# Optimization experiments

Measured on AMD Instinct MI355X. Metric: run time of the kernel, lower is better.

Reference implementation:

```python
import jax, jax.numpy as jnp
import numpy as np

N_NODES = 100000
N_EDGES = 1600000
K = 48

def setup_inputs() -> dict:
    key = jax.random.key(0)
    ks = jax.random.split(key, 6)
    x = jax.random.normal(ks[0], (N_NODES, K), dtype=jnp.float32)
    pos_edge_index = jax.random.randint(ks[1], (2, N_EDGES), 0, N_NODES, dtype=jnp.int64)
    neg_edge_index = jax.random.randint(ks[2], (2, N_EDGES), 0, N_NODES, dtype=jnp.int64)
    # nn.Linear-style init (uniform +-1/sqrt(fan_in))
    lim1 = 1.0 / np.sqrt(3 * K)
    W1 = jax.random.uniform(ks[3], (3 * K, 16), minval=-lim1, maxval=lim1, dtype=jnp.float32)
    b1 = jnp.zeros((16,), dtype=jnp.float32)
    lim2 = 1.0 / np.sqrt(16)
    W2 = jax.random.uniform(ks[4], (16, K), minval=-lim2, maxval=lim2, dtype=jnp.float32)
    b2 = jnp.zeros((K,), dtype=jnp.float32)
    return {"x": x, "pos_edge_index": pos_edge_index, "neg_edge_index": neg_edge_index,
            "W1": W1, "b1": b1, "W2": W2, "b2": b2}

def _scatter_add_mp(x, edge_index):
    # PyG MessagePassing(aggr='add'), message = x_j:
    # gather source-node features and scatter-add into target nodes.
    src, dst = edge_index[0], edge_index[1]
    msgs = x[src]  # [E, k]
    return jax.ops.segment_sum(msgs, dst, num_segments=x.shape[0])  # [N, k]

def reference(x, pos_edge_index, neg_edge_index, W1, b1, W2, b2):
    x_pos = _scatter_add_mp(x, pos_edge_index)
    x_neg = _scatter_add_mp(x, neg_edge_index)
    out_cat = jnp.concatenate([x, x_pos, x_neg], axis=1)  # [N, 3k]
    h = jnp.tanh(out_cat @ W1 + b1)                        # [N, 16]
    C = h @ W2 + b2                                        # [N, k]
    return jax.nn.softmax(C, axis=1)
```

## Files before the change

### kernel.cpp

```cpp
#include <hip/hip_runtime.h>
#include <hip/hip_fp16.h>
#include <math.h>

#define NN 100000
#define NE 1600000
#define KF 48
#define NEDGE_ALL (2 * NE)

#define BKT_NODES 128
#define NBKT_PER  782
#define NBKT      1564
#define PACK_EPB  16384
#define STG_HALF  8192
#define NPB       196
#define OT2       1566
#define CAP2      2432
#define KSTG      10

typedef _Float16 half2v __attribute__((ext_vector_type(2)));
typedef _Float16 half4v __attribute__((ext_vector_type(4)));
typedef _Float16 half8v __attribute__((ext_vector_type(8)));

#if defined(__has_builtin)
#if __has_builtin(__builtin_amdgcn_fdot2)
#define HAVE_FDOT2 1
#endif
#endif

__device__ __forceinline__ void acc_pair(float& ax, float& ay, half2v v)
{
#ifdef HAVE_FDOT2
    ax = __builtin_amdgcn_fdot2(v, (half2v){(_Float16)1.f, (_Float16)0.f}, ax, false);
    ay = __builtin_amdgcn_fdot2(v, (half2v){(_Float16)0.f, (_Float16)1.f}, ay, false);
#else
    ax += (float)v.x;
    ay += (float)v.y;
#endif
}

__global__ __launch_bounds__(512) void pack_kernel(
    const float* __restrict__ x,
    const int* __restrict__ ei_pos,
    const int* __restrict__ ei_neg,
    const float* __restrict__ W1,
    const float* __restrict__ b1,
    unsigned short* __restrict__ offT,
    unsigned* __restrict__ plist,
    float* __restrict__ za,
    __half* __restrict__ zbh,
    __half* __restrict__ zch)
{
    __shared__ int cnt[NBKT];
    __shared__ int ps[391];
    __shared__ unsigned stage[STG_HALF];
    __shared__ float sW1[144 * 16];
    __shared__ float sb1[16];

    const int t = threadIdx.x;
    for (int i = t; i < 144 * 16; i += 512) sW1[i] = W1[i];
    if (t < 16) sb1[t] = b1[t];
    for (int i = t; i < NBKT; i += 512) cnt[i] = 0;
    __syncthreads();

    {
        const int n = blockIdx.x * 512 + t;
        if (n < NN + 2) {
            float aA[16], aB[16], aC[16];
#pragma unroll
            for (int j = 0; j < 16; ++j) { aA[j] = sb1[j]; aB[j] = 0.f; aC[j] = 0.f; }
            if (n < NN) {
                const float4* __restrict__ x4 = (const float4*)(x + (long)n * KF);
                for (int i4 = 0; i4 < 12; ++i4) {
                    float4 v = x4[i4];
                    float vv[4] = {v.x, v.y, v.z, v.w};
#pragma unroll
                    for (int c = 0; c < 4; ++c) {
                        const int f = i4 * 4 + c;
                        const float* wA = &sW1[f * 16];
                        const float* wB = &sW1[(48 + f) * 16];
                        const float* wC = &sW1[(96 + f) * 16];
                        const float s = vv[c];
#pragma unroll
                        for (int j = 0; j < 16; ++j) {
                            aA[j] += s * wA[j];
                            aB[j] += s * wB[j];
                            aC[j] += s * wC[j];
                        }
                    }
                }
                float4* za4 = (float4*)(za + (long)n * 16);
#pragma unroll
                for (int j4 = 0; j4 < 4; ++j4)
                    za4[j4] = make_float4(aA[4*j4], aA[4*j4+1], aA[4*j4+2], aA[4*j4+3]);
            }
            half8v hb0, hb1, hc0, hc1;
#pragma unroll
            for (int j = 0; j < 8; ++j) {
                hb0[j] = (_Float16)aB[j];     hb1[j] = (_Float16)aB[8 + j];
                hc0[j] = (_Float16)aC[j];     hc1[j] = (_Float16)aC[8 + j];
            }
            half8v* zb8 = (half8v*)zbh;
            half8v* zc8 = (half8v*)zch;
            zb8[(long)n * 2 + 0] = hb0;  zb8[(long)n * 2 + 1] = hb1;
            zc8[(long)n * 2 + 0] = hc0;  zc8[(long)n * 2 + 1] = hc1;
        }
    }

    unsigned pk[32];
    int bk[32];
    const int blockBase = blockIdx.x * PACK_EPB;
#pragma unroll
    for (int j = 0; j < 32; ++j) {
        int e = blockBase + j * 512 + t;
        bk[j] = -1;
        if (e < NEDGE_ALL) {
            int list = e >= NE;
            int ee = list ? e - NE : e;
            const int* ei = list ? ei_neg : ei_pos;
            int src = ei[ee];
            int dst = ei[NE + ee];
            int b = list * NBKT_PER + (dst >> 7);
            bk[j] = b;
            pk[j] = ((unsigned)(dst & 127) << 17) | (unsigned)src;
            atomicAdd(&cnt[b], 1);
        }
    }
    __syncthreads();

    int s0 = 0, s1 = 0, s2 = 0, s3 = 0;
    if (t < 391) {
        s0 = cnt[4 * t]; s1 = cnt[4 * t + 1]; s2 = cnt[4 * t + 2]; s3 = cnt[4 * t + 3];
        ps[t] = s0 + s1 + s2 + s3;
    }
    __syncthreads();
    for (int d = 1; d < 391; d <<= 1) {
        int v = (t < 391 && t >= d) ? ps[t - d] : 0;
        __syncthreads();
        if (t < 391) ps[t] += v;
        __syncthreads();
    }
    unsigned short* myrow = offT + (long)blockIdx.x * OT2;
    if (t < 391) {
        int base = t ? ps[t - 1] : 0;
        int o0 = base, o1 = o0 + s0, o2 = o1 + s1, o3 = o2 + s2;
        myrow[4 * t]     = (unsigned short)o0;
        myrow[4 * t + 1] = (unsigned short)o1;
        myrow[4 * t + 2] = (unsigned short)o2;
        myrow[4 * t + 3] = (unsigned short)o3;
        cnt[4 * t] = o0; cnt[4 * t + 1] = o1; cnt[4 * t + 2] = o2; cnt[4 * t + 3] = o3;
    }
    if (t == 390) myrow[NBKT] = (unsigned short)ps[390];
    __syncthreads();

#pragma unroll
    for (int j = 0; j < 32; ++j) {
        if (bk[j] >= 0)
            bk[j] = atomicAdd(&cnt[bk[j]], 1);
    }

#pragma unroll
    for (int j = 0; j < 32; ++j) {
        if (bk[j] >= 0 && bk[j] < STG_HALF)
            stage[bk[j]] = pk[j];
    }
    __syncthreads();
    {
        const uint4* __restrict__ st4 = (const uint4*)stage;
        uint4* __restrict__ out4 = (uint4*)(plist + (long)blockIdx.x * PACK_EPB);
#pragma unroll
        for (int j = 0; j < 4; ++j)
            out4[j * 512 + t] = st4[j * 512 + t];
    }
    __syncthreads();

#pragma unroll
    for (int j = 0; j < 32; ++j) {
        if (bk[j] >= STG_HALF)
            stage[bk[j] - STG_HALF] = pk[j];
    }
    __syncthreads();
    {
        const uint4* __restrict__ st4 = (const uint4*)stage;
        uint4* __restrict__ out4 = (uint4*)(plist + (long)blockIdx.x * PACK_EPB + STG_HALF);
#pragma unroll
        for (int j = 0; j < 4; ++j)
            out4[j * 512 + t] = st4[j * 512 + t];
    }
}

__global__ __launch_bounds__(256) void gather_kernel(
    const __half* __restrict__ zbh,
    const __half* __restrict__ zch,
    const unsigned* __restrict__ plist,
    const unsigned short* __restrict__ offT,
    float* __restrict__ hpos,
    float* __restrict__ hneg)
{
    __shared__ unsigned srt[CAP2];
    __shared__ int rb[NPB + 2];
    __shared__ int sc[NPB];
    __shared__ unsigned short rsL[NPB];
    __shared__ int nh[BKT_NODES];
    __shared__ int starts[BKT_NODES];
    __shared__ int ends[BKT_NODES];
    __shared__ int cur2[BKT_NODES];

    const int b = blockIdx.x;
    const int t = threadIdx.x;

    if (t < NPB) {
        int s = offT[(long)t * OT2 + b];
        int e = offT[(long)t * OT2 + b + 1];
        rsL[t] = (unsigned short)s;
        sc[t] = e - s;
    }
    if (t < BKT_NODES) nh[t] = 0;
    __syncthreads();

    for (int d = 1; d < NPB; d <<= 1) {
        int v = (t < NPB && t >= d) ? sc[t - d] : 0;
        __syncthreads();
        if (t < NPB) sc[t] += v;
        __syncthreads();
    }
    if (t < NPB) rb[t + 1] = sc[t];
    if (t == 0) rb[0] = 0;
    __syncthreads();
    int cb = rb[NPB];
    if (cb > CAP2) cb = CAP2;

    unsigned held[KSTG];
#pragma unroll
    for (int k = 0; k < KSTG; ++k) {
        int i = t + k * 256;
        held[k] = 0;
        if (i < cb) {
            int lo = 0, hi = NPB - 1;
#pragma unroll
            for (int it = 0; it < 8; ++it) {
                int mid = (lo + hi + 1) >> 1;
                bool ge = (rb[mid] <= i);
                lo = ge ? mid : lo;
                hi = ge ? hi : mid - 1;
            }
            unsigned p = plist[(long)lo * PACK_EPB + rsL[lo] + (i - rb[lo])];
            held[k] = p;
            atomicAdd(&nh[p >> 17], 1);
        }
    }
    __syncthreads();

    for (int d = 1; d < BKT_NODES; d <<= 1) {
        int v = 0;
        if (t < BKT_NODES && t >= d) v = nh[t - d];
        __syncthreads();
        if (t < BKT_NODES) nh[t] += v;
        __syncthreads();
    }
    if (t < BKT_NODES) {
        int e_ = min(nh[t], CAP2);
        int s_ = t ? min(nh[t - 1], CAP2) : 0;
        starts[t] = s_;
        ends[t] = e_;
        cur2[t] = s_;
    }
    __syncthreads();

#pragma unroll
    for (int k = 0; k < KSTG; ++k) {
        int i = t + k * 256;
        if (i < cb) {
            unsigned p = held[k];
            int slot = atomicAdd(&cur2[p >> 17], 1);
            if (slot < CAP2) srt[slot] = p;
        }
    }
    __syncthreads();

    const int wave = t >> 6, lane = t & 63;
    const int g = lane >> 2;
    const int sub = lane & 3;
    const int list = b >= NBKT_PER;
    const int nb = list ? b - NBKT_PER : b;
    float* o = list ? hneg : hpos;
    const half4v* __restrict__ z4 = (const half4v*)(list ? zch : zbh);

    for (int n = wave; n < BKT_NODES; n += 4) {
        int gn = nb * BKT_NODES + n;
        if (gn >= NN) continue;
        int s = starts[n], e = ends[n];
        float a0 = 0.f, a1 = 0.f, a2 = 0.f, a3 = 0.f;
        for (int j = s; j < e; j += 16) {
            int i0 = j + g;
            int q = (i0 < e) ? (int)(srt[i0 < CAP2 ? i0 : 0] & 0x1FFFFu) : NN;
            half4v v = z4[q * 4 + sub];
            acc_pair(a0, a1, (half2v){v.x, v.y});
            acc_pair(a2, a3, (half2v){v.z, v.w});
        }
        a0 += __shfl_xor(a0, 4); a0 += __shfl_xor(a0, 8); a0 += __shfl_xor(a0, 16); a0 += __shfl_xor(a0, 32);
        a1 += __shfl_xor(a1, 4); a1 += __shfl_xor(a1, 8); a1 += __shfl_xor(a1, 16); a1 += __shfl_xor(a1, 32);
        a2 += __shfl_xor(a2, 4); a2 += __shfl_xor(a2, 8); a2 += __shfl_xor(a2, 16); a2 += __shfl_xor(a2, 32);
        a3 += __shfl_xor(a3, 4); a3 += __shfl_xor(a3, 8); a3 += __shfl_xor(a3, 16); a3 += __shfl_xor(a3, 32);
        if (g == 0) {
            float4* o4 = (float4*)o;
            o4[(long)gn * 4 + sub] = make_float4(a0, a1, a2, a3);
        }
    }
}

__global__ __launch_bounds__(256) void mlp2_kernel(
    const float* __restrict__ za,
    const float* __restrict__ hpos,
    const float* __restrict__ hneg,
    const float* __restrict__ W2,
    const float* __restrict__ b2,
    float* __restrict__ out)
{
    __shared__ float sW2[16 * 48];
    __shared__ float sb2[48];
    for (int i = threadIdx.x; i < 16 * 48; i += 256) sW2[i] = W2[i];
    if (threadIdx.x < 48) sb2[threadIdx.x] = b2[threadIdx.x];
    __syncthreads();

    const int n = blockIdx.x * 256 + threadIdx.x;
    if (n >= NN) return;

    const float4* A = (const float4*)(za   + (long)n * 16);
    const float4* P = (const float4*)(hpos + (long)n * 16);
    const float4* Q = (const float4*)(hneg + (long)n * 16);
    float h[16];
#pragma unroll
    for (int j4 = 0; j4 < 4; ++j4) {
        float4 a = A[j4], p = P[j4], q = Q[j4];
        h[4 * j4 + 0] = tanhf(a.x + p.x + q.x);
        h[4 * j4 + 1] = tanhf(a.y + p.y + q.y);
        h[4 * j4 + 2] = tanhf(a.z + p.z + q.z);
        h[4 * j4 + 3] = tanhf(a.w + p.w + q.w);
    }

    float C[KF];
#pragma unroll
    for (int k = 0; k < KF; ++k) C[k] = sb2[k];
    for (int j = 0; j < 16; ++j) {
        const float hv = h[j];
        const float* w = &sW2[j * KF];
#pragma unroll
        for (int k = 0; k < KF; ++k) C[k] += hv * w[k];
    }

    float m = C[0];
#pragma unroll
    for (int k = 1; k < KF; ++k) m = fmaxf(m, C[k]);
    float ssum = 0.f;
#pragma unroll
    for (int k = 0; k < KF; ++k) { C[k] = expf(C[k] - m); ssum += C[k]; }
    const float inv = 1.0f / ssum;

    float4* po = (float4*)(out + (long)n * KF);
#pragma unroll
    for (int k4 = 0; k4 < 12; ++k4)
        po[k4] = make_float4(C[4*k4] * inv, C[4*k4+1] * inv, C[4*k4+2] * inv, C[4*k4+3] * inv);
}

__global__ __launch_bounds__(256) void scatter2_kernel(
    const float* __restrict__ x,
    const int* __restrict__ ei_pos,
    const int* __restrict__ ei_neg,
    float* acc_pos,
    float* acc_neg)
{
    const int list = blockIdx.y;
    const int* ei = list ? ei_neg : ei_pos;
    float* acc = list ? acc_neg : acc_pos;

    long t = (long)blockIdx.x * blockDim.x + threadIdx.x;
    const long total = (long)NE * 12;
    if (t >= total) return;

    int e = (int)(t / 12);
    int r = (int)(t - (long)e * 12);
    int k4 = r * 4;

    int src = ei[e];
    int dst = ei[NE + e];

    const float4 v = *(const float4*)(x + (long)src * KF + k4);
    float* p = acc + (long)dst * KF + k4;

    unsafeAtomicAdd(p + 0, v.x);
    unsafeAtomicAdd(p + 1, v.y);
    unsafeAtomicAdd(p + 2, v.z);
    unsafeAtomicAdd(p + 3, v.w);
}

__global__ __launch_bounds__(256) void mlp_softmax_kernel(
    const float* __restrict__ x,
    const float* xpos,
    const float* __restrict__ xneg,
    const float* __restrict__ W1,
    const float* __restrict__ b1,
    const float* __restrict__ W2,
    const float* __restrict__ b2,
    float* out)
{
    __shared__ float sW1[144 * 16];
    __shared__ float sW2[16 * 48];
    __shared__ float sb1[16];
    __shared__ float sb2[48];

    for (int i = threadIdx.x; i < 144 * 16; i += blockDim.x) sW1[i] = W1[i];
    for (int i = threadIdx.x; i < 16 * 48;  i += blockDim.x) sW2[i] = W2[i];
    if (threadIdx.x < 16) sb1[threadIdx.x] = b1[threadIdx.x];
    if (threadIdx.x < 48) sb2[threadIdx.x] = b2[threadIdx.x];
    __syncthreads();

    const int n = blockIdx.x * blockDim.x + threadIdx.x;
    if (n >= NN) return;

    float h[16];
#pragma unroll
    for (int j = 0; j < 16; ++j) h[j] = sb1[j];

    const float* srcs[3];
    srcs[0] = x    + (long)n * KF;
    srcs[1] = xpos + (long)n * KF;
    srcs[2] = xneg + (long)n * KF;

    for (int s = 0; s < 3; ++s) {
        const float* px = srcs[s];
        for (int i = 0; i < KF; ++i) {
            const float v = px[i];
            const float* w = &sW1[(s * KF + i) * 16];
#pragma unroll
            for (int j = 0; j < 16; ++j) h[j] += v * w[j];
        }
    }
#pragma unroll
    for (int j = 0; j < 16; ++j) h[j] = tanhf(h[j]);

    float C[KF];
#pragma unroll
    for (int k = 0; k < KF; ++k) C[k] = sb2[k];
    for (int j = 0; j < 16; ++j) {
        const float hv = h[j];
        const float* w = &sW2[j * KF];
#pragma unroll
        for (int k = 0; k < KF; ++k) C[k] += hv * w[k];
    }

    float m = C[0];
#pragma unroll
    for (int k = 1; k < KF; ++k) m = fmaxf(m, C[k]);
    float ssum = 0.f;
#pragma unroll
    for (int k = 0; k < KF; ++k) { C[k] = expf(C[k] - m); ssum += C[k]; }
    const float inv = 1.0f / ssum;

    float* po = out + (long)n * KF;
#pragma unroll
    for (int k = 0; k < KF; ++k) po[k] = C[k] * inv;
}

extern "C" void kernel_launch(void* const* d_in, const int* in_sizes, int n_in,
                              void* d_out, int out_size, void* d_ws, size_t ws_size,
                              hipStream_t stream)
{
    const float* x      = (const float*)d_in[0];
    const int*   ei_pos = (const int*)  d_in[1];
    const int*   ei_neg = (const int*)  d_in[2];
    const float* W1     = (const float*)d_in[3];
    const float* b1     = (const float*)d_in[4];
    const float* W2     = (const float*)d_in[5];
    const float* b2     = (const float*)d_in[6];

    float* out = (float*)d_out;

    const size_t h_bytes     = (size_t)NN * 16 * sizeof(float);
    const size_t za_bytes    = (size_t)NN * 16 * sizeof(float);
    const size_t zh_bytes    = (size_t)(NN + 2) * 16 * sizeof(__half);
    const size_t plist_bytes = (size_t)NPB * PACK_EPB * sizeof(unsigned);
    const size_t offT_bytes  = (size_t)NPB * OT2 * sizeof(unsigned short);

    size_t off = 0;
    char* ws = (char*)d_ws;
    float*          hpos  = (float*)(ws + off);          off += h_bytes;
    float*          hneg  = (float*)(ws + off);          off += h_bytes;
    float*          za    = (float*)(ws + off);          off += za_bytes;
    __half*         zbh   = (__half*)(ws + off);         off += zh_bytes;
    __half*         zch   = (__half*)(ws + off);         off += zh_bytes;
    unsigned*       plist = (unsigned*)(ws + off);       off += plist_bytes;
    unsigned short* offT  = (unsigned short*)(ws + off); off += offT_bytes;
    const size_t needed = off;

    if (ws_size >= needed) {
        pack_kernel<<<NPB, 512, 0, stream>>>(x, ei_pos, ei_neg, W1, b1, offT, plist, za, zbh, zch);
        gather_kernel<<<NBKT, 256, 0, stream>>>(zbh, zch, plist, offT, hpos, hneg);
        mlp2_kernel<<<(NN + 255) / 256, 256, 0, stream>>>(za, hpos, hneg, W2, b2, out);
    } else {
        float* xpos = (float*)d_out;
        float* xneg = (float*)d_ws;
        const size_t acc_bytes = (size_t)NN * KF * sizeof(float);
        hipMemsetAsync(xpos, 0, acc_bytes, stream);
        hipMemsetAsync(xneg, 0, acc_bytes, stream);
        const long total = (long)NE * 12;
        dim3 grid((unsigned)((total + 255) / 256), 2, 1);
        scatter2_kernel<<<grid, 256, 0, stream>>>(x, ei_pos, ei_neg, xpos, xneg);
        mlp_softmax_kernel<<<(NN + 255) / 256, 256, 0, stream>>>(x, xpos, xneg, W1, b1, W2, b2, out);
    }
}
```

Measured before the change: 207.2 us.

## Transpose bucket offset table and remap gather blocks across XCDs by list

Adds a small transpose kernel that turns the per-pack-block offset table into a bucket-major layout, so each gather block reads its 196 start/end offsets contiguously instead of with a large stride. The gather grid is also remapped so blocks on XCDs 0-3 handle the positive list and XCDs 4-7 the negative list. The aim is to keep each half-precision feature table in fewer L2 caches and to coalesce the offset loads. The cost is an extra kernel launch and some padded blocks that return immediately.

```diff
diff --git a/kernel.cpp b/kernel.cpp
--- a/kernel.cpp
+++ b/kernel.cpp
@@ -14,6 +14,7 @@
 #define STG_HALF  8192
 #define NPB       196
 #define OT2       1566
+#define OTT       200
 #define CAP2      2432
 #define KSTG      10
 
@@ -188,11 +189,34 @@
     }
 }
 
+__global__ __launch_bounds__(256) void transposeT_kernel(
+    const unsigned short* __restrict__ offT,
+    unsigned short* __restrict__ offTT)
+{
+    __shared__ unsigned short tile[64][NPB + 6];
+    const int t = threadIdx.x;
+    const int b0 = blockIdx.x * 64;
+
+    for (int idx = t; idx < 64 * NPB; idx += 256) {
+        int r = idx >> 6;
+        int c = idx & 63;
+        int b = b0 + c;
+        tile[c][r] = (b <= NBKT) ? offT[(long)r * OT2 + b] : (unsigned short)0;
+    }
+    __syncthreads();
+    for (int idx = t; idx < 64 * NPB; idx += 256) {
+        int c = idx / NPB;
+        int r = idx - c * NPB;
+        int b = b0 + c;
+        if (b <= NBKT) offTT[(long)b * OTT + r] = tile[c][r];
+    }
+}
+
 __global__ __launch_bounds__(256) void gather_kernel(
     const __half* __restrict__ zbh,
     const __half* __restrict__ zch,
     const unsigned* __restrict__ plist,
-    const unsigned short* __restrict__ offT,
+    const unsigned short* __restrict__ offTT,
     float* __restrict__ hpos,
     float* __restrict__ hneg)
 {
@@ -205,12 +229,19 @@
     __shared__ int ends[BKT_NODES];
     __shared__ int cur2[BKT_NODES];
 
-    const int b = blockIdx.x;
+    const int bid = blockIdx.x;
+    const int xcd = bid & 7;
+    const int slot = bid >> 3;
+    const int list = xcd >> 2;
+    const int nb = slot * 4 + (xcd & 3);
+    if (nb >= NBKT_PER) return;
+    const int b = list * NBKT_PER + nb;
+
     const int t = threadIdx.x;
 
     if (t < NPB) {
-        int s = offT[(long)t * OT2 + b];
-        int e = offT[(long)t * OT2 + b + 1];
+        int s = offTT[(long)b * OTT + t];
+        int e = offTT[(long)(b + 1) * OTT + t];
         rsL[t] = (unsigned short)s;
         sc[t] = e - s;
     }
@@ -271,8 +302,8 @@
         int i = t + k * 256;
         if (i < cb) {
             unsigned p = held[k];
-            int slot = atomicAdd(&cur2[p >> 17], 1);
-            if (slot < CAP2) srt[slot] = p;
+            int slot2 = atomicAdd(&cur2[p >> 17], 1);
+            if (slot2 < CAP2) srt[slot2] = p;
         }
     }
     __syncthreads();
@@ -280,8 +311,6 @@
     const int wave = t >> 6, lane = t & 63;
     const int g = lane >> 2;
     const int sub = lane & 3;
-    const int list = b >= NBKT_PER;
-    const int nb = list ? b - NBKT_PER : b;
     float* o = list ? hneg : hpos;
     const half4v* __restrict__ z4 = (const half4v*)(list ? zch : zbh);
 
@@ -480,6 +509,7 @@
     const size_t zh_bytes    = (size_t)(NN + 2) * 16 * sizeof(__half);
     const size_t plist_bytes = (size_t)NPB * PACK_EPB * sizeof(unsigned);
     const size_t offT_bytes  = (size_t)NPB * OT2 * sizeof(unsigned short);
+    const size_t offTT_bytes = (size_t)(NBKT + 2) * OTT * sizeof(unsigned short);
 
     size_t off = 0;
     char* ws = (char*)d_ws;
@@ -490,11 +520,13 @@
     __half*         zch   = (__half*)(ws + off);         off += zh_bytes;
     unsigned*       plist = (unsigned*)(ws + off);       off += plist_bytes;
     unsigned short* offT  = (unsigned short*)(ws + off); off += offT_bytes;
+    unsigned short* offTT = (unsigned short*)(ws + off); off += offTT_bytes;
     const size_t needed = off;
 
     if (ws_size >= needed) {
         pack_kernel<<<NPB, 512, 0, stream>>>(x, ei_pos, ei_neg, W1, b1, offT, plist, za, zbh, zch);
-        gather_kernel<<<NBKT, 256, 0, stream>>>(zbh, zch, plist, offT, hpos, hneg);
+        transposeT_kernel<<<(NBKT + 1 + 63) / 64, 256, 0, stream>>>(offT, offTT);
+        gather_kernel<<<196 * 8, 256, 0, stream>>>(zbh, zch, plist, offTT, hpos, hneg);
         mlp2_kernel<<<(NN + 255) / 256, 256, 0, stream>>>(za, hpos, hneg, W2, b2, out);
     } else {
         float* xpos = (float*)d_out;
```

Result: slower. 223.4 us (+7.8%).

## Fuse gather and MLP/softmax into one kernel with transposed offset table

Applied to the files above, without the earlier changes.

Merges the gather and final MLP/softmax kernels so each block processes both positive and negative lists for its 128-node bucket, accumulating hidden pre-activations in shared memory instead of writing hpos/hneg to global memory. The offset table is transposed so gather blocks read contiguous offsets, and the per-edge binary search is replaced by a shared run-id lookup table. This halves the gather grid (782 blocks doing two passes each), which lowers parallelism and may reduce latency hiding on the irregular gather.

```diff
diff --git a/kernel.cpp b/kernel.cpp
--- a/kernel.cpp
+++ b/kernel.cpp
@@ -13,7 +13,7 @@
 #define PACK_EPB  16384
 #define STG_HALF  8192
 #define NPB       196
-#define OT2       1566
+#define OTT       200
 #define CAP2      2432
 #define KSTG      10
 
@@ -44,7 +44,7 @@
     const int* __restrict__ ei_neg,
     const float* __restrict__ W1,
     const float* __restrict__ b1,
-    unsigned short* __restrict__ offT,
+    unsigned short* __restrict__ offTT,
     unsigned* __restrict__ plist,
     float* __restrict__ za,
     __half* __restrict__ zbh,
@@ -139,17 +139,17 @@
         if (t < 391) ps[t] += v;
         __syncthreads();
     }
-    unsigned short* myrow = offT + (long)blockIdx.x * OT2;
+    const int r = blockIdx.x;
     if (t < 391) {
         int base = t ? ps[t - 1] : 0;
         int o0 = base, o1 = o0 + s0, o2 = o1 + s1, o3 = o2 + s2;
-        myrow[4 * t]     = (unsigned short)o0;
-        myrow[4 * t + 1] = (unsigned short)o1;
-        myrow[4 * t + 2] = (unsigned short)o2;
-        myrow[4 * t + 3] = (unsigned short)o3;
+        offTT[(long)(4 * t)     * OTT + r] = (unsigned short)o0;
+        offTT[(long)(4 * t + 1) * OTT + r] = (unsigned short)o1;
+        offTT[(long)(4 * t + 2) * OTT + r] = (unsigned short)o2;
+        offTT[(long)(4 * t + 3) * OTT + r] = (unsigned short)o3;
         cnt[4 * t] = o0; cnt[4 * t + 1] = o1; cnt[4 * t + 2] = o2; cnt[4 * t + 3] = o3;
     }
-    if (t == 390) myrow[NBKT] = (unsigned short)ps[390];
+    if (t == 390) offTT[(long)NBKT * OTT + r] = (unsigned short)ps[390];
     __syncthreads();
 
 #pragma unroll
@@ -188,178 +188,177 @@
     }
 }
 
-__global__ __launch_bounds__(256) void gather_kernel(
+__global__ __launch_bounds__(256) void gather_fused_kernel(
     const __half* __restrict__ zbh,
     const __half* __restrict__ zch,
     const unsigned* __restrict__ plist,
-    const unsigned short* __restrict__ offT,
-    float* __restrict__ hpos,
-    float* __restrict__ hneg)
+    const unsigned short* __restrict__ offTT,
+    const float* __restrict__ za,
+    const float* __restrict__ W2,
+    const float* __restrict__ b2,
+    float* __restrict__ out)
 {
     __shared__ unsigned srt[CAP2];
     __shared__ int rb[NPB + 2];
     __shared__ int sc[NPB];
     __shared__ unsigned short rsL[NPB];
+    __shared__ unsigned char runid[CAP2];
     __shared__ int nh[BKT_NODES];
     __shared__ int starts[BKT_NODES];
     __shared__ int ends[BKT_NODES];
     __shared__ int cur2[BKT_NODES];
-
-    const int b = blockIdx.x;
-    const int t = threadIdx.x;
-
-    if (t < NPB) {
-        int s = offT[(long)t * OT2 + b];
-        int e = offT[(long)t * OT2 + b + 1];
-        rsL[t] = (unsigned short)s;
-        sc[t] = e - s;
-    }
-    if (t < BKT_NODES) nh[t] = 0;
-    __syncthreads();
-
-    for (int d = 1; d < NPB; d <<= 1) {
-        int v = (t < NPB && t >= d) ? sc[t - d] : 0;
-        __syncthreads();
-        if (t < NPB) sc[t] += v;
-        __syncthreads();
-    }
-    if (t < NPB) rb[t + 1] = sc[t];
-    if (t == 0) rb[0] = 0;
-    __syncthreads();
-    int cb = rb[NPB];
-    if (cb > CAP2) cb = CAP2;
-
-    unsigned held[KSTG];
-#pragma unroll
-    for (int k = 0; k < KSTG; ++k) {
-        int i = t + k * 256;
-        held[k] = 0;
-        if (i < cb) {
-            int lo = 0, hi = NPB - 1;
-#pragma unroll
-            for (int it = 0; it < 8; ++it) {
-                int mid = (lo + hi + 1) >> 1;
-                bool ge = (rb[mid] <= i);
-                lo = ge ? mid : lo;
-                hi = ge ? hi : mid - 1;
-            }
-            unsigned p = plist[(long)lo * PACK_EPB + rsL[lo] + (i - rb[lo])];
-            held[k] = p;
-            atomicAdd(&nh[p >> 17], 1);
-        }
-    }
-    __syncthreads();
-
-    for (int d = 1; d < BKT_NODES; d <<= 1) {
-        int v = 0;
-        if (t < BKT_NODES && t >= d) v = nh[t - d];
-        __syncthreads();
-        if (t < BKT_NODES) nh[t] += v;
-        __syncthreads();
-    }
-    if (t < BKT_NODES) {
-        int e_ = min(nh[t], CAP2);
-        int s_ = t ? min(nh[t - 1], CAP2) : 0;
-        starts[t] = s_;
-        ends[t] = e_;
-        cur2[t] = s_;
-    }
-    __syncthreads();
-
-#pragma unroll
-    for (int k = 0; k < KSTG; ++k) {
-        int i = t + k * 256;
-        if (i < cb) {
-            unsigned p = held[k];
-            int slot = atomicAdd(&cur2[p >> 17], 1);
-            if (slot < CAP2) srt[slot] = p;
-        }
-    }
-    __syncthreads();
-
-    const int wave = t >> 6, lane = t & 63;
-    const int g = lane >> 2;
-    const int sub = lane & 3;
-    const int list = b >= NBKT_PER;
-    const int nb = list ? b - NBKT_PER : b;
-    float* o = list ? hneg : hpos;
-    const half4v* __restrict__ z4 = (const half4v*)(list ? zch : zbh);
-
-    for (int n = wave; n < BKT_NODES; n += 4) {
-        int gn = nb * BKT_NODES + n;
-        if (gn >= NN) continue;
-        int s = starts[n], e = ends[n];
-        float a0 = 0.f, a1 = 0.f, a2 = 0.f, a3 = 0.f;
-        for (int j = s; j < e; j += 16) {
-            int i0 = j + g;
-            int q = (i0 < e) ? (int)(srt[i0 < CAP2 ? i0 : 0] & 0x1FFFFu) : NN;
-            half4v v = z4[q * 4 + sub];
-            acc_pair(a0, a1, (half2v){v.x, v.y});
-            acc_pair(a2, a3, (half2v){v.z, v.w});
-        }
-        a0 += __shfl_xor(a0, 4); a0 += __shfl_xor(a0, 8); a0 += __shfl_xor(a0, 16); a0 += __shfl_xor(a0, 32);
-        a1 += __shfl_xor(a1, 4); a1 += __shfl_xor(a1, 8); a1 += __shfl_xor(a1, 16); a1 += __shfl_xor(a1, 32);
-        a2 += __shfl_xor(a2, 4); a2 += __shfl_xor(a2, 8); a2 += __shfl_xor(a2, 16); a2 += __shfl_xor(a2, 32);
-        a3 += __shfl_xor(a3, 4); a3 += __shfl_xor(a3, 8); a3 += __shfl_xor(a3, 16); a3 += __shfl_xor(a3, 32);
-        if (g == 0) {
-            float4* o4 = (float4*)o;
-            o4[(long)gn * 4 + sub] = make_float4(a0, a1, a2, a3);
-        }
-    }
-}
-
-__global__ __launch_bounds__(256) void mlp2_kernel(
-    const float* __restrict__ za,
-    const float* __restrict__ hpos,
-    const float* __restrict__ hneg,
-    const float* __restrict__ W2,
-    const float* __restrict__ b2,
-    float* __restrict__ out)
-{
+    __shared__ float hbuf[BKT_NODES][17];
     __shared__ float sW2[16 * 48];
     __shared__ float sb2[48];
-    for (int i = threadIdx.x; i < 16 * 48; i += 256) sW2[i] = W2[i];
-    if (threadIdx.x < 48) sb2[threadIdx.x] = b2[threadIdx.x];
-    __syncthreads();
-
-    const int n = blockIdx.x * 256 + threadIdx.x;
-    if (n >= NN) return;
-
-    const float4* A = (const float4*)(za   + (long)n * 16);
-    const float4* P = (const float4*)(hpos + (long)n * 16);
-    const float4* Q = (const float4*)(hneg + (long)n * 16);
-    float h[16];
-#pragma unroll
-    for (int j4 = 0; j4 < 4; ++j4) {
-        float4 a = A[j4], p = P[j4], q = Q[j4];
-        h[4 * j4 + 0] = tanhf(a.x + p.x + q.x);
-        h[4 * j4 + 1] = tanhf(a.y + p.y + q.y);
-        h[4 * j4 + 2] = tanhf(a.z + p.z + q.z);
-        h[4 * j4 + 3] = tanhf(a.w + p.w + q.w);
-    }
-
-    float C[KF];
-#pragma unroll
-    for (int k = 0; k < KF; ++k) C[k] = sb2[k];
-    for (int j = 0; j < 16; ++j) {
-        const float hv = h[j];
-        const float* w = &sW2[j * KF];
-#pragma unroll
-        for (int k = 0; k < KF; ++k) C[k] += hv * w[k];
-    }
-
-    float m = C[0];
-#pragma unroll
-    for (int k = 1; k < KF; ++k) m = fmaxf(m, C[k]);
-    float ssum = 0.f;
-#pragma unroll
-    for (int k = 0; k < KF; ++k) { C[k] = expf(C[k] - m); ssum += C[k]; }
-    const float inv = 1.0f / ssum;
-
-    float4* po = (float4*)(out + (long)n * KF);
-#pragma unroll
-    for (int k4 = 0; k4 < 12; ++k4)
-        po[k4] = make_float4(C[4*k4] * inv, C[4*k4+1] * inv, C[4*k4+2] * inv, C[4*k4+3] * inv);
+
+    const int nb = blockIdx.x;
+    const int t = threadIdx.x;
+
+    for (int i = t; i < 16 * 48; i += 256) sW2[i] = W2[i];
+    if (t < 48) sb2[t] = b2[t];
+    for (int i = t; i < BKT_NODES * 17; i += 256) ((float*)hbuf)[i] = 0.f;
+
+    for (int list = 0; list < 2; ++list) {
+        const int b = list * NBKT_PER + nb;
+        __syncthreads();
+
+        if (t < NPB) {
+            int s = offTT[(long)b * OTT + t];
+            int e = offTT[(long)(b + 1) * OTT + t];
+            rsL[t] = (unsigned short)s;
+            sc[t] = e - s;
+        }
+        if (t < BKT_NODES) nh[t] = 0;
+        __syncthreads();
+
+        for (int d = 1; d < NPB; d <<= 1) {
+            int v = (t < NPB && t >= d) ? sc[t - d] : 0;
+            __syncthreads();
+            if (t < NPB) sc[t] += v;
+            __syncthreads();
+        }
+        if (t < NPB) rb[t + 1] = sc[t];
+        if (t == 0) rb[0] = 0;
+        __syncthreads();
+        int cb = rb[NPB];
+        if (cb > CAP2) cb = CAP2;
+
+        if (t < NPB) {
+            int s_ = min(rb[t], cb);
+            int e_ = min(rb[t + 1], cb);
+            for (int j = s_; j < e_; ++j) runid[j] = (unsigned char)t;
+        }
+        __syncthreads();
+
+        unsigned held[KSTG];
+#pragma unroll
+        for (int k = 0; k < KSTG; ++k) {
+            int i = t + k * 256;
+            held[k] = 0;
+            if (i < cb) {
+                int lo = (int)runid[i];
+                unsigned p = plist[(long)lo * PACK_EPB + rsL[lo] + (i - rb[lo])];
+                held[k] = p;
+                atomicAdd(&nh[p >> 17], 1);
+            }
+        }
+        __syncthreads();
+
+        for (int d = 1; d < BKT_NODES; d <<= 1) {
+            int v = 0;
+            if (t < BKT_NODES && t >= d) v = nh[t - d];
+            __syncthreads();
+            if (t < BKT_NODES) nh[t] += v;
+            __syncthreads();
+        }
+        if (t < BKT_NODES) {
+            int e_ = min(nh[t], CAP2);
+            int s_ = t ? min(nh[t - 1], CAP2) : 0;
+            starts[t] = s_;
+            ends[t] = e_;
+            cur2[t] = s_;
+        }
+        __syncthreads();
+
+#pragma unroll
+        for (int k = 0; k < KSTG; ++k) {
+            int i = t + k * 256;
+            if (i < cb) {
+                unsigned p = held[k];
+                int sl = atomicAdd(&cur2[p >> 17], 1);
+                if (sl < CAP2) srt[sl] = p;
+            }
+        }
+        __syncthreads();
+
+        const int wave = t >> 6, lane = t & 63;
+        const int g = lane >> 2;
+        const int sub = lane & 3;
+        const half4v* __restrict__ z4 = (const half4v*)(list ? zch : zbh);
+
+        for (int n = wave; n < BKT_NODES; n += 4) {
+            int s = starts[n], e = ends[n];
+            float a0 = 0.f, a1 = 0.f, a2 = 0.f, a3 = 0.f;
+            for (int j = s; j < e; j += 16) {
+                int i0 = j + g;
+                int q = (i0 < e) ? (int)(srt[i0 < CAP2 ? i0 : 0] & 0x1FFFFu) : NN;
+                half4v v = z4[q * 4 + sub];
+                acc_pair(a0, a1, (half2v){v.x, v.y});
+                acc_pair(a2, a3, (half2v){v.z, v.w});
+            }
+            a0 += __shfl_xor(a0, 4); a0 += __shfl_xor(a0, 8); a0 += __shfl_xor(a0, 16); a0 += __shfl_xor(a0, 32);
+            a1 += __shfl_xor(a1, 4); a1 += __shfl_xor(a1, 8); a1 += __shfl_xor(a1, 16); a1 += __shfl_xor(a1, 32);
+            a2 += __shfl_xor(a2, 4); a2 += __shfl_xor(a2, 8); a2 += __shfl_xor(a2, 16); a2 += __shfl_xor(a2, 32);
+            a3 += __shfl_xor(a3, 4); a3 += __shfl_xor(a3, 8); a3 += __shfl_xor(a3, 16); a3 += __shfl_xor(a3, 32);
+            if (g == 0) {
+                hbuf[n][4 * sub + 0] += a0;
+                hbuf[n][4 * sub + 1] += a1;
+                hbuf[n][4 * sub + 2] += a2;
+                hbuf[n][4 * sub + 3] += a3;
+            }
+        }
+    }
+    __syncthreads();
+
+    if (t < BKT_NODES) {
+        const int gn = nb * BKT_NODES + t;
+        if (gn < NN) {
+            float h[16];
+            const float4* A = (const float4*)(za + (long)gn * 16);
+#pragma unroll
+            for (int j4 = 0; j4 < 4; ++j4) {
+                float4 a = A[j4];
+                h[4 * j4 + 0] = tanhf(a.x + hbuf[t][4 * j4 + 0]);
+                h[4 * j4 + 1] = tanhf(a.y + hbuf[t][4 * j4 + 1]);
+                h[4 * j4 + 2] = tanhf(a.z + hbuf[t][4 * j4 + 2]);
+                h[4 * j4 + 3] = tanhf(a.w + hbuf[t][4 * j4 + 3]);
+            }
+
+            float C[KF];
+#pragma unroll
+            for (int k = 0; k < KF; ++k) C[k] = sb2[k];
+            for (int j = 0; j < 16; ++j) {
+                const float hv = h[j];
+                const float* w = &sW2[j * KF];
+#pragma unroll
+                for (int k = 0; k < KF; ++k) C[k] += hv * w[k];
+            }
+
+            float m = C[0];
+#pragma unroll
+            for (int k = 1; k < KF; ++k) m = fmaxf(m, C[k]);
+            float ssum = 0.f;
+#pragma unroll
+            for (int k = 0; k < KF; ++k) { C[k] = expf(C[k] - m); ssum += C[k]; }
+            const float inv = 1.0f / ssum;
+
+            float4* po = (float4*)(out + (long)gn * KF);
+#pragma unroll
+            for (int k4 = 0; k4 < 12; ++k4)
+                po[k4] = make_float4(C[4*k4] * inv, C[4*k4+1] * inv,
+                                     C[4*k4+2] * inv, C[4*k4+3] * inv);
+        }
+    }
 }
 
 __global__ __launch_bounds__(256) void scatter2_kernel(
@@ -475,27 +474,23 @@
 
     float* out = (float*)d_out;
 
-    const size_t h_bytes     = (size_t)NN * 16 * sizeof(float);
     const size_t za_bytes    = (size_t)NN * 16 * sizeof(float);
     const size_t zh_bytes    = (size_t)(NN + 2) * 16 * sizeof(__half);
     const size_t plist_bytes = (size_t)NPB * PACK_EPB * sizeof(unsigned);
-    const size_t offT_bytes  = (size_t)NPB * OT2 * sizeof(unsigned short);
+    const size_t offTT_bytes = (size_t)(NBKT + 2) * OTT * sizeof(unsigned short);
 
     size_t off = 0;
     char* ws = (char*)d_ws;
-    float*          hpos  = (float*)(ws + off);          off += h_bytes;
-    float*          hneg  = (float*)(ws + off);          off += h_bytes;
     float*          za    = (float*)(ws + off);          off += za_bytes;
     __half*         zbh   = (__half*)(ws + off);         off += zh_bytes;
     __half*         zch   = (__half*)(ws + off);         off += zh_bytes;
     unsigned*       plist = (unsigned*)(ws + off);       off += plist_bytes;
-    unsigned short* offT  = (unsigned short*)(ws + off); off += offT_bytes;
+    unsigned short* offTT = (unsigned short*)(ws + off); off += offTT_bytes;
     const size_t needed = off;
 
     if (ws_size >= needed) {
-        pack_kernel<<<NPB, 512, 0, stream>>>(x, ei_pos, ei_neg, W1, b1, offT, plist, za, zbh, zch);
-        gather_kernel<<<NBKT, 256, 0, stream>>>(zbh, zch, plist, offT, hpos, hneg);
-        mlp2_kernel<<<(NN + 255) / 256, 256, 0, stream>>>(za, hpos, hneg, W2, b2, out);
+        pack_kernel<<<NPB, 512, 0, stream>>>(x, ei_pos, ei_neg, W1, b1, offTT, plist, za, zbh, zch);
+        gather_fused_kernel<<<NBKT_PER, 256, 0, stream>>>(zbh, zch, plist, offTT, za, W2, b2, out);
     } else {
         float* xpos = (float*)d_out;
         float* xneg = (float*)d_ws;
```

Measured after the change: 222.6 us. 7.4% more time.
